# Kernel tuning notes

Hardware: AMD Instinct MI355X
Metric: run time of the kernel (lower is better)

The kernel has to match this reference:

```python
import jax, jax.numpy as jnp
import numpy as np

B, CIN, COUT, T, S = 4, 32, 64, 8, 3   # batch, in-ch, out-ch, num_taps, stencil edge
D, H, W = 32, 64, 64                    # input volume
PAD = 1                                 # zero padding (stride 1) -> same spatial output


def setup_inputs() -> dict:
    key = jax.random.key(0)
    k1, k2, k3, k4 = jax.random.split(key, 4)
    x = jax.random.normal(k1, (B, CIN, D, H, W), jnp.float32)
    stencils = jax.random.normal(k2, (B, T, S, S, S), jnp.float32)
    weight = jax.random.normal(k3, (COUT, CIN, T), jnp.float32) * 0.05
    bias = jax.random.normal(k4, (COUT,), jnp.float32) * 0.05
    return {"x": x, "stencils": stencils, "weight": weight, "bias": bias}


def reference(x, stencils, weight, bias):
    # x: (B,Cin,D,H,W); stencils: (B,T,sx,sy,sz); weight: (Cout,Cin,T); bias: (Cout,)
    b, cin = x.shape[:2]
    t = stencils.shape[1]
    sx, sy, sz = stencils.shape[2:]
    # zero-pad spatially
    xp = jnp.pad(x, ((0, 0), (0, 0), (PAD, PAD), (PAD, PAD), (PAD, PAD)))
    # fold batch into channels -> grouped conv with groups = B*Cin (per-sample stencils)
    x_exp = xp.reshape(1, b * cin, xp.shape[2], xp.shape[3], xp.shape[4])
    # per-sample stencils shared across Cin, one output feature per (b, cin, tap)
    w = jnp.broadcast_to(stencils[:, None], (b, cin, t, sx, sy, sz))
    w = w.reshape(b * cin * t, 1, sx, sy, sz)
    tap = jax.lax.conv_general_dilated(
        x_exp, w,
        window_strides=(1, 1, 1), padding='VALID',
        dimension_numbers=('NCDHW', 'OIDHW', 'NCDHW'),
        feature_group_count=b * cin,
    )  # (1, B*Cin*T, Do, Ho, Wo)
    do, ho, wo = tap.shape[-3:]
    tap = tap.reshape(b, cin, t, do, ho, wo)
    # channel/tap mixing: (B,Cin,T,D,H,W) x (Cout,Cin,T) -> (B,Cout,D,H,W)
    y = jnp.einsum('bctdhw,oct->bodhw', tap, weight)
    return y + bias[None, :, None, None, None]
```

## Files before the change

### kernel.cpp

```cpp
#include <hip/hip_runtime.h>

typedef short bf16x8 __attribute__((ext_vector_type(8)));
typedef float f32x16 __attribute__((ext_vector_type(16)));

typedef const __attribute__((address_space(1))) unsigned int GUint;
typedef __attribute__((address_space(3))) unsigned int LUint;

#define XT_BYTES 37914624ull
#define XROW 2176

__device__ __forceinline__ unsigned short f2bf(float f) {
    unsigned u = __float_as_uint(f);
    return (unsigned short)((u + 0x7FFFu + ((u >> 16) & 1u)) >> 16);
}

__global__ __launch_bounds__(256) void prep_x(const float* __restrict__ x,
                                              uint4* __restrict__ xt) {
    int yp = blockIdx.x;
    int zp = blockIdx.y;
    int b  = blockIdx.z;
    int t  = threadIdx.x;
    size_t rowbase = ((((size_t)b * 34 + zp) * 66 + yp) * 66) * 4;
    bool in_zy = (zp >= 1 && zp <= 32 && yp >= 1 && yp <= 64);
    for (int idx = t; idx < 264; idx += 256) {
        int q = idx & 3, xp = idx >> 2;
        uint4 v = make_uint4(0u, 0u, 0u, 0u);
        if (in_zy && xp >= 1 && xp <= 64) {
            int d = zp - 1, h = yp - 1, w = xp - 1;
            const float* xb = x + ((((size_t)b * 32 + q * 8) * 32 + d) * 64 + h) * 64 + w;
            unsigned short us[8];
            #pragma unroll
            for (int j = 0; j < 8; ++j)
                us[j] = f2bf(xb[(size_t)j * 131072]);
            v.x = us[0] | ((unsigned)us[1] << 16);
            v.y = us[2] | ((unsigned)us[3] << 16);
            v.z = us[4] | ((unsigned)us[5] << 16);
            v.w = us[6] | ((unsigned)us[7] << 16);
        }
        int pos = q ^ ((xp >> 1) & 3);
        xt[rowbase + (size_t)xp * 4 + pos] = v;
    }
}

__global__ __launch_bounds__(256) void prep_keff(const float* __restrict__ stencils,
                                                 const float* __restrict__ weight,
                                                 uint4* __restrict__ kf2) {
    int i = blockIdx.x * 256 + threadIdx.x;
    if (i >= 27648) return;
    int lane = i & 63;
    int mt = (i >> 6) & 1;
    int s  = (i >> 7) & 1;
    int br = i >> 8;
    int r = br % 27, b = br / 27;
    int o  = (lane & 31) + 32 * mt;
    int cb = s * 16 + (lane >> 5) * 8;
    float st[8];
    #pragma unroll
    for (int t = 0; t < 8; ++t) st[t] = stencils[((size_t)b * 8 + t) * 27 + r];
    unsigned short us[8];
    #pragma unroll
    for (int j = 0; j < 8; ++j) {
        const float* wp = weight + ((size_t)o * 32 + cb + j) * 8;
        float acc = 0.f;
        #pragma unroll
        for (int t = 0; t < 8; ++t) acc += wp[t] * st[t];
        us[j] = f2bf(acc);
    }
    uint4 v;
    v.x = us[0] | ((unsigned)us[1] << 16);
    v.y = us[2] | ((unsigned)us[3] << 16);
    v.z = us[4] | ((unsigned)us[5] << 16);
    v.w = us[6] | ((unsigned)us[7] << 16);
    kf2[i] = v;
}

__global__ __launch_bounds__(256, 2) void conv_mfma(
    const uint4* __restrict__ xt, const uint4* __restrict__ kf2,
    const float* __restrict__ bias, float* __restrict__ out) {
    __shared__ __align__(1024) char smem[52224];

    int n = blockIdx.x;
    int xcd = n & 7, local = n >> 3;
    int dt = local & 15;
    int cmb = (local >> 4) | (xcd << 4);
    int ht = cmb & 15, wt = (cmb >> 4) & 1, b = cmb >> 5;

    int tid = threadIdx.x;
    int lane = tid & 63, wid = tid >> 6;
    int nlo = lane & 31, kh = lane >> 5;

    const char* xtc = (const char*)xt;

    for (int row = wid; row < 24; row += 4) {
        int z = row / 6, yy = row - z * 6;
        size_t gbase = ((((size_t)b * 34 + dt * 2 + z) * 66 + ht * 4 + yy) * 66 + wt * 32) * 64;
        int ldsbase = row * XROW;
        #pragma unroll
        for (int cb = 0; cb < 136; cb += 64) {
            int rem = 136 - cb;
            if (lane < rem) {
                __builtin_amdgcn_global_load_lds(
                    (GUint*)(xtc + gbase + (size_t)(cb + lane) * 16),
                    (LUint*)(smem + ldsbase + cb * 16), 16, 0, 0);
            }
        }
    }

    int z = wid >> 1;
    int ys = (wid & 1) << 1;

    int Badr[2][3];
    #pragma unroll
    for (int s = 0; s < 2; ++s)
        #pragma unroll
        for (int k3 = 0; k3 < 3; ++k3) {
            int xl = nlo + k3;
            int pos = (s * 2 + kh) ^ ((xl >> 1) & 3);
            Badr[s][k3] = (z * 6 + ys) * XROW + xl * 64 + (pos << 4);
        }

    const uint4* kfb = kf2 + (size_t)b * 27 * 256 + lane;

    bf16x8 aCur[4], aNxt[4];
    #pragma unroll
    for (int fi = 0; fi < 4; ++fi)
        aCur[fi] = *(const bf16x8*)(kfb + fi * 64);

    f32x16 acc[2][2];
    #pragma unroll
    for (int mt = 0; mt < 2; ++mt)
        #pragma unroll
        for (int nt = 0; nt < 2; ++nt)
            #pragma unroll
            for (int e = 0; e < 16; ++e) acc[mt][nt][e] = 0.f;

    __syncthreads();

    #pragma unroll
    for (int r = 0; r < 27; ++r) {
        const int i3 = r / 9, j3 = (r / 3) % 3, k3 = r % 3;
        if (r < 26) {
            #pragma unroll
            for (int fi = 0; fi < 4; ++fi)
                aNxt[fi] = *(const bf16x8*)(kfb + ((r + 1) * 4 + fi) * 64);
        }
        #pragma unroll
        for (int s = 0; s < 2; ++s) {
            #pragma unroll
            for (int nt = 0; nt < 2; ++nt) {
                bf16x8 bb = *(const bf16x8*)(smem + (i3 * 6 + j3 + nt) * XROW + Badr[s][k3]);
                acc[0][nt] = __builtin_amdgcn_mfma_f32_32x32x16_bf16(aCur[s * 2 + 0], bb, acc[0][nt], 0, 0, 0);
                acc[1][nt] = __builtin_amdgcn_mfma_f32_32x32x16_bf16(aCur[s * 2 + 1], bb, acc[1][nt], 0, 0, 0);
            }
        }
        if (r < 26) {
            #pragma unroll
            for (int fi = 0; fi < 4; ++fi) aCur[fi] = aNxt[fi];
        }
    }

    int d = dt * 2 + z, w = wt * 32 + nlo;
    #pragma unroll
    for (int mt = 0; mt < 2; ++mt) {
        #pragma unroll
        for (int nt = 0; nt < 2; ++nt) {
            int h = ht * 4 + ys + nt;
            size_t sp = (((size_t)d) * 64 + h) * 64 + w;
            #pragma unroll
            for (int reg = 0; reg < 16; ++reg) {
                int o = mt * 32 + (reg & 3) + 8 * (reg >> 2) + 4 * kh;
                out[(((size_t)(b * 64 + o)) << 17) + sp] = acc[mt][nt][reg] + bias[o];
            }
        }
    }
}

extern "C" void kernel_launch(void* const* d_in, const int* in_sizes, int n_in,
                              void* d_out, int out_size, void* d_ws, size_t ws_size,
                              hipStream_t stream) {
    const float* x        = (const float*)d_in[0];
    const float* stencils = (const float*)d_in[1];
    const float* weight   = (const float*)d_in[2];
    const float* bias     = (const float*)d_in[3];
    float* out = (float*)d_out;

    uint4* xtbuf = (uint4*)d_ws;
    uint4* kf2   = (uint4*)((char*)d_ws + XT_BYTES);

    prep_x<<<dim3(66, 34, 4), 256, 0, stream>>>(x, xtbuf);
    prep_keff<<<108, 256, 0, stream>>>(stencils, weight, kf2);
    conv_mfma<<<2048, 256, 0, stream>>>(xtbuf, kf2, bias, out);
}
```

Before: 252.8 us.

## Fuse input bf16 transpose/pad into conv kernel's LDS staging

Removes the separate prep_x kernel, which wrote a padded channel-last bf16 copy of x to workspace. The conv kernel now reads fp32 x directly, converts it to bf16, handles padding with bounds checks, and writes the swizzled tile into LDS. This drops a kernel launch and a full write-then-read round trip of the transformed volume. In exchange, halo regions are re-read from fp32 global memory by neighbouring blocks, the 8-channel gather uses strided scalar loads, and the async global_load_lds path is replaced by synchronous loads plus LDS stores.

```diff
diff --git a/kernel.cpp b/kernel.cpp
--- a/kernel.cpp
+++ b/kernel.cpp
@@ -3,43 +3,11 @@
 typedef short bf16x8 __attribute__((ext_vector_type(8)));
 typedef float f32x16 __attribute__((ext_vector_type(16)));
 
-typedef const __attribute__((address_space(1))) unsigned int GUint;
-typedef __attribute__((address_space(3))) unsigned int LUint;
-
-#define XT_BYTES 37914624ull
 #define XROW 2176
 
 __device__ __forceinline__ unsigned short f2bf(float f) {
     unsigned u = __float_as_uint(f);
     return (unsigned short)((u + 0x7FFFu + ((u >> 16) & 1u)) >> 16);
-}
-
-__global__ __launch_bounds__(256) void prep_x(const float* __restrict__ x,
-                                              uint4* __restrict__ xt) {
-    int yp = blockIdx.x;
-    int zp = blockIdx.y;
-    int b  = blockIdx.z;
-    int t  = threadIdx.x;
-    size_t rowbase = ((((size_t)b * 34 + zp) * 66 + yp) * 66) * 4;
-    bool in_zy = (zp >= 1 && zp <= 32 && yp >= 1 && yp <= 64);
-    for (int idx = t; idx < 264; idx += 256) {
-        int q = idx & 3, xp = idx >> 2;
-        uint4 v = make_uint4(0u, 0u, 0u, 0u);
-        if (in_zy && xp >= 1 && xp <= 64) {
-            int d = zp - 1, h = yp - 1, w = xp - 1;
-            const float* xb = x + ((((size_t)b * 32 + q * 8) * 32 + d) * 64 + h) * 64 + w;
-            unsigned short us[8];
-            #pragma unroll
-            for (int j = 0; j < 8; ++j)
-                us[j] = f2bf(xb[(size_t)j * 131072]);
-            v.x = us[0] | ((unsigned)us[1] << 16);
-            v.y = us[2] | ((unsigned)us[3] << 16);
-            v.z = us[4] | ((unsigned)us[5] << 16);
-            v.w = us[6] | ((unsigned)us[7] << 16);
-        }
-        int pos = q ^ ((xp >> 1) & 3);
-        xt[rowbase + (size_t)xp * 4 + pos] = v;
-    }
 }
 
 __global__ __launch_bounds__(256) void prep_keff(const float* __restrict__ stencils,
@@ -74,8 +42,8 @@
     kf2[i] = v;
 }
 
-__global__ __launch_bounds__(256, 2) void conv_mfma(
-    const uint4* __restrict__ xt, const uint4* __restrict__ kf2,
+__global__ __launch_bounds__(256, 2) void conv_fused(
+    const float* __restrict__ x, const uint4* __restrict__ kf2,
     const float* __restrict__ bias, float* __restrict__ out) {
     __shared__ __align__(1024) char smem[52224];
 
@@ -89,21 +57,26 @@
     int lane = tid & 63, wid = tid >> 6;
     int nlo = lane & 31, kh = lane >> 5;
 
-    const char* xtc = (const char*)xt;
-
-    for (int row = wid; row < 24; row += 4) {
+    for (int task = tid; task < 3264; task += 256) {
+        int row = task / 136;
+        int chunk = task - row * 136;
+        int q = chunk & 3, xp = chunk >> 2;
         int z = row / 6, yy = row - z * 6;
-        size_t gbase = ((((size_t)b * 34 + dt * 2 + z) * 66 + ht * 4 + yy) * 66 + wt * 32) * 64;
-        int ldsbase = row * XROW;
-        #pragma unroll
-        for (int cb = 0; cb < 136; cb += 64) {
-            int rem = 136 - cb;
-            if (lane < rem) {
-                __builtin_amdgcn_global_load_lds(
-                    (GUint*)(xtc + gbase + (size_t)(cb + lane) * 16),
-                    (LUint*)(smem + ldsbase + cb * 16), 16, 0, 0);
-            }
+        int gd = dt * 2 + z - 1, gh = ht * 4 + yy - 1, gw = wt * 32 + xp - 1;
+        uint4 v = make_uint4(0u, 0u, 0u, 0u);
+        if ((unsigned)gd < 32u && (unsigned)gh < 64u && (unsigned)gw < 64u) {
+            const float* xb = x + (((size_t)(b * 32 + q * 8) * 32 + gd) * 64 + gh) * 64 + gw;
+            unsigned short us[8];
+            #pragma unroll
+            for (int j = 0; j < 8; ++j)
+                us[j] = f2bf(xb[(size_t)j * 131072]);
+            v.x = us[0] | ((unsigned)us[1] << 16);
+            v.y = us[2] | ((unsigned)us[3] << 16);
+            v.z = us[4] | ((unsigned)us[5] << 16);
+            v.w = us[6] | ((unsigned)us[7] << 16);
         }
+        int pos = q ^ ((xp >> 1) & 3);
+        *(uint4*)(smem + row * XROW + xp * 64 + (pos << 4)) = v;
     }
 
     int z = wid >> 1;
@@ -184,10 +157,8 @@
     const float* bias     = (const float*)d_in[3];
     float* out = (float*)d_out;
 
-    uint4* xtbuf = (uint4*)d_ws;
-    uint4* kf2   = (uint4*)((char*)d_ws + XT_BYTES);
+    uint4* kf2 = (uint4*)d_ws;
 
-    prep_x<<<dim3(66, 34, 4), 256, 0, stream>>>(x, xtbuf);
     prep_keff<<<108, 256, 0, stream>>>(stencils, weight, kf2);
-    conv_mfma<<<2048, 256, 0, stream>>>(xtbuf, kf2, bias, out);
+    conv_fused<<<2048, 256, 0, stream>>>(x, kf2, bias, out);
 }
```

Measured after the change: 250.7 us. Within noise of the previous version (-0.8%).
